# Performance work log

Hardware: AMD Instinct MI355X
Metric: run time of the kernel (lower is better)

## Reference

```python
import jax, jax.numpy as jnp
import numpy as np

INPUT_DIM = 512
HIDDEN_DIM = 512
B, N = 8, 2048


def setup_inputs() -> dict:
    key = jax.random.key(0)
    ks = jax.random.split(key, 9)
    s_in = 1.0 / np.sqrt(INPUT_DIM)
    s_h = 1.0 / np.sqrt(HIDDEN_DIM)
    return {
        "X": jax.random.normal(ks[0], (B, N, INPUT_DIM), dtype=jnp.float32),
        "Wq": jax.random.uniform(ks[1], (INPUT_DIM, HIDDEN_DIM), minval=-s_in, maxval=s_in),
        "bq": jnp.zeros((HIDDEN_DIM,), jnp.float32),
        "Wk": jax.random.uniform(ks[2], (INPUT_DIM, HIDDEN_DIM), minval=-s_in, maxval=s_in),
        "bk": jnp.zeros((HIDDEN_DIM,), jnp.float32),
        "Wv": jax.random.uniform(ks[3], (INPUT_DIM, HIDDEN_DIM), minval=-s_in, maxval=s_in),
        "bv": jnp.zeros((HIDDEN_DIM,), jnp.float32),
        "Wo": jax.random.uniform(ks[4], (HIDDEN_DIM, INPUT_DIM), minval=-s_h, maxval=s_h),
        "bo": jnp.zeros((INPUT_DIM,), jnp.float32),
        "ln_gamma": jnp.ones((INPUT_DIM,), jnp.float32),
        "ln_beta": jnp.zeros((INPUT_DIM,), jnp.float32),
    }


def reference(X, Wq, bq, Wk, bk, Wv, bv, Wo, bo, ln_gamma, ln_beta):
    q = X @ Wq + bq                      # [B,N,H]
    k = X @ Wk + bk
    v = X @ Wv + bv
    scores = jnp.einsum('bnh,bmh->bnm', q, k) / jnp.sqrt(jnp.float32(HIDDEN_DIM))
    attn = jax.nn.softmax(scores, axis=-1)      # [B,N,N]
    ctx = jnp.einsum('bnm,bmh->bnh', attn, v)   # [B,N,H]
    out = ctx @ Wo + bo + X                      # residual
    mu = jnp.mean(out, axis=-1, keepdims=True)
    var = jnp.var(out, axis=-1, keepdims=True)
    normed = (out - mu) / jnp.sqrt(var + 1e-5)
    return normed * ln_gamma + ln_beta
```

## Files before the change

### kernel.cpp

```cpp
#include <hip/hip_runtime.h>
#include <cstdint>
#include <cstddef>


typedef __bf16 bf16x8 __attribute__((ext_vector_type(8)));
typedef float  f32x4  __attribute__((ext_vector_type(4)));

__device__ __forceinline__ uint16_t f2bf(float f) {
  union { float f; uint32_t u; } v; v.f = f;
  uint32_t r = v.u + 0x7FFFu + ((v.u >> 16) & 1u);
  return (uint16_t)(r >> 16);
}

__device__ __forceinline__ void gld16(const uint16_t* g, uint16_t* l) {
  __builtin_amdgcn_global_load_lds(
      (__attribute__((address_space(1))) void*)(g),
      (__attribute__((address_space(3))) void*)(l), 16, 0, 0);
}

template <int MODE, int BM, int BN>
__global__ __launch_bounds__(512, 2) void gemm2_k(
    const uint16_t* __restrict__ A, const uint16_t* __restrict__ Bt,
    void* __restrict__ OutA, uint16_t* __restrict__ OutK,
    uint16_t* __restrict__ OutVT, float* __restrict__ rsum, int K, int lda,
    int ldb, const float* __restrict__ b0, const float* __restrict__ b1,
    const float* __restrict__ b2, float scale) {
  constexpr int MT = (BM / 2) / 16;
  constexpr int NT = (BN / 4) / 16;
  constexpr int AI = BM / 64;
  constexpr int BI = BN / 64;
  static_assert(NT == 4, "BN must be 256");
  __shared__ alignas(16) uint16_t As[2][BM * 64];
  __shared__ alignas(16) uint16_t Bs[2][BN * 64];

  const int tid = threadIdx.x;
  const int w = tid >> 6, lane = tid & 63;
  const int wm = w >> 2, wn = w & 3;

  const int gx = gridDim.x, gy = gridDim.y;
  const int nwg = gx * gy * gridDim.z;
  const int hw = blockIdx.x + gx * (blockIdx.y + gy * blockIdx.z);
  const int lg = (hw & 7) * (nwg >> 3) + (hw >> 3);
  const int bx = lg % gx, byz = lg / gx;
  const int by = byz % gy, z = byz / gy;

  const int m0 = by * BM, n0 = bx * BN;

  const uint16_t* Ab = A;
  const uint16_t* Bb = Bt;
  if (MODE == 1) { Ab += (size_t)z * 2048 * 512;  Bb += (size_t)z * 2048 * 512; }
  if (MODE == 2) { Ab += (size_t)z * 2048 * 2048; Bb += (size_t)z * 512 * 2048; }

  const int l3 = lane >> 3, l7 = lane & 7;
  const int csw = (l7 ^ l3) * 8;
  const uint16_t* gA = Ab + (size_t)(m0 + w * (BM / 8) + l3) * lda + csw;
  const uint16_t* gB = Bb + (size_t)(n0 + w * (BN / 8) + l3) * ldb + csw;

  auto stage = [&](int t, int b) {
    const int k0 = t * 64;
#pragma unroll
    for (int j = 0; j < AI; j++)
      gld16(gA + k0 + (size_t)(j * 8) * lda,
            &As[b][(w * (BM / 8) + j * 8) * 64]);
#pragma unroll
    for (int j = 0; j < BI; j++)
      gld16(gB + k0 + (size_t)(j * 8) * ldb,
            &Bs[b][(w * (BN / 8) + j * 8) * 64]);
  };

  f32x4 acc[MT][NT];
#pragma unroll
  for (int i = 0; i < MT; i++)
#pragma unroll
    for (int j = 0; j < NT; j++) acc[i][j] = (f32x4){0.f, 0.f, 0.f, 0.f};

  const int lr = lane & 15, q4 = lane >> 4;
  const int rc0 = ((q4) ^ (lr & 7)) * 8;
  const int rc1 = ((4 + q4) ^ (lr & 7)) * 8;

  const int NK = K >> 6;

  stage(0, 0);
  asm volatile("s_waitcnt vmcnt(0)" ::: "memory");
  __builtin_amdgcn_s_barrier();

  int cur = 0;
  for (int t = 0; t < NK; ++t) {
    if (t + 1 < NK) stage(t + 1, cur ^ 1);
#pragma unroll
    for (int ks = 0; ks < 2; ks++) {
      const int rc = ks ? rc1 : rc0;
      bf16x8 af[MT], bfr[NT];
#pragma unroll
      for (int mt = 0; mt < MT; mt++)
        af[mt] = *(const bf16x8*)
            &As[cur][(wm * (BM / 2) + mt * 16 + lr) * 64 + rc];
#pragma unroll
      for (int nt = 0; nt < NT; nt++)
        bfr[nt] = *(const bf16x8*)&Bs[cur][(wn * 64 + nt * 16 + lr) * 64 + rc];
#pragma unroll
      for (int nt = 0; nt < NT; nt++)
#pragma unroll
        for (int mt = 0; mt < MT; mt++)
          acc[mt][nt] = __builtin_amdgcn_mfma_f32_16x16x32_bf16(
              af[mt], bfr[nt], acc[mt][nt], 0, 0, 0);
    }
    if (t + 1 < NK) {
      asm volatile("s_waitcnt lgkmcnt(0)" ::: "memory");
      asm volatile("s_waitcnt vmcnt(0)" ::: "memory");
      __builtin_amdgcn_s_barrier();
      cur ^= 1;
    }
  }

  if (MODE == 1) {
    uint16_t* Sp = (uint16_t*)OutA + (size_t)z * 2048 * 2048;
#pragma unroll
    for (int mt = 0; mt < MT; mt++) {
      float rp[4] = {0.f, 0.f, 0.f, 0.f};
#pragma unroll
      for (int nt = 0; nt < NT; nt++) {
#pragma unroll
        for (int i = 0; i < 4; i++) {
          const int row = m0 + wm * (BM / 2) + mt * 16 + q4 * 4 + i;
          const int col = n0 + wn * 64 + nt * 16 + lr;
          const float e = __expf(acc[mt][nt][i] * scale);
          Sp[(size_t)row * 2048 + col] = f2bf(e);
          rp[i] += e;
        }
      }
#pragma unroll
      for (int i = 0; i < 4; i++) {
        float p = rp[i];
        p += __shfl_xor(p, 1); p += __shfl_xor(p, 2);
        p += __shfl_xor(p, 4); p += __shfl_xor(p, 8);
        if (lr == 0) {
          const int row = m0 + wm * (BM / 2) + mt * 16 + q4 * 4 + i;
          atomicAdd(&rsum[z * 2048 + row], p);
        }
      }
    }
  } else if (MODE == 2) {
#pragma unroll
    for (int mt = 0; mt < MT; mt++) {
#pragma unroll
      for (int i = 0; i < 4; i++) {
        const int row = m0 + wm * (BM / 2) + mt * 16 + q4 * 4 + i;
        const float sc = 1.0f / rsum[z * 2048 + row];
#pragma unroll
        for (int nt = 0; nt < NT; nt++) {
          const int col = n0 + wn * 64 + nt * 16 + lr;
          ((uint16_t*)OutA)[((size_t)z * 2048 + row) * 512 + col] =
              f2bf(acc[mt][nt][i] * sc);
        }
      }
    }
  } else {
#pragma unroll
    for (int mt = 0; mt < MT; mt++) {
#pragma unroll
      for (int nt = 0; nt < NT; nt++) {
#pragma unroll
        for (int i = 0; i < 4; i++) {
          const int row = m0 + wm * (BM / 2) + mt * 16 + q4 * 4 + i;
          const int col = n0 + wn * 64 + nt * 16 + lr;
          const float v = acc[mt][nt][i];
          const int which = col >> 9, c = col & 511;
          if (which == 0) {
            ((uint16_t*)OutA)[(size_t)row * 512 + c] = f2bf(v + b0[c]);
          } else if (which == 1) {
            OutK[(size_t)row * 512 + c] = f2bf(v + b1[c]);
          } else {
            OutVT[(size_t)(row >> 11) * (512 * 2048) + (size_t)c * 2048 +
                  (row & 2047)] = f2bf(v + b2[c]);
          }
        }
      }
    }
  }
}

template <int MODE, int BM, int BN, int WM, int WN>
__global__ __launch_bounds__(512, 4) void gemm_k(
    const uint16_t* __restrict__ A, const uint16_t* __restrict__ Bt,
    void* __restrict__ OutA, float* __restrict__ rsum, int K, int lda,
    int ldb, const float* __restrict__ b0, const float* __restrict__ b1,
    const float* __restrict__ b2, const float* __restrict__ Xres) {
  constexpr int MT = (BM / WM) / 16;
  constexpr int NT = (BN / WN) / 16;
  static_assert(MT == 4 && NT == 4, "wave tile must be 64x64");
  constexpr int AI = (BM >= 128) ? BM / 128 : 1;
  constexpr int BI = BN / 128;
  constexpr int PW = AI + BI;
  __shared__ alignas(16) uint16_t As[3][BM * 32];
  __shared__ alignas(16) uint16_t Bs[3][BN * 32];

  const int tid = threadIdx.x;
  const int w = tid >> 6, lane = tid & 63;
  const int wm = w / WN, wn = w % WN;

  const int gx = gridDim.x, gy = gridDim.y;
  const int nwg = gx * gy * gridDim.z;
  const int hw = blockIdx.x + gx * (blockIdx.y + gy * blockIdx.z);
  const int lg = (hw & 7) * (nwg >> 3) + (hw >> 3);
  const int bx = lg % gx, byz = lg / gx;
  const int by = byz % gy;

  const int m0 = by * BM, n0 = bx * BN;

  const uint16_t* Ab = A;
  const uint16_t* Bb = Bt;

  const int kc = (((lane & 3) ^ ((lane >> 2) & 3) ^ (lane >> 4)) * 8);
  const int rbA = (BM >= 128) ? w * (BM / 8) : (w & 3) * 16;
  const int rbB = w * (BN / 8);
  const uint16_t* gA = Ab + (size_t)(m0 + rbA + (lane >> 2)) * lda + kc;
  const uint16_t* gB = Bb + (size_t)(n0 + rbB + (lane >> 2)) * ldb + kc;

  f32x4 acc[MT][NT];
#pragma unroll
  for (int i = 0; i < MT; i++)
#pragma unroll
    for (int j = 0; j < NT; j++) acc[i][j] = (f32x4){0.f, 0.f, 0.f, 0.f};

  const int lr = lane & 15, q4 = lane >> 4;
  const int swz = (((lane >> 4) ^ (lr & 3) ^ (lr >> 2)) * 8);
  const int iters = K >> 5;

  auto stage = [&](int t, int buf) {
    const int k0 = t * 32;
#pragma unroll
    for (int j = 0; j < AI; j++)
      gld16(gA + k0 + (size_t)(j * 16) * lda, &As[buf][(rbA + j * 16) * 32]);
#pragma unroll
    for (int j = 0; j < BI; j++)
      gld16(gB + k0 + (size_t)(j * 16) * ldb, &Bs[buf][(rbB + j * 16) * 32]);
  };

  auto compute = [&](int buf) {
    bf16x8 af[MT], bfr[NT];
#pragma unroll
    for (int t = 0; t < MT; t++)
      af[t] = *(const bf16x8*)&As[buf][(wm * (BM / WM) + t * 16 + lr) * 32 + swz];
#pragma unroll
    for (int t = 0; t < NT; t++)
      bfr[t] = *(const bf16x8*)&Bs[buf][(wn * (BN / WN) + t * 16 + lr) * 32 + swz];
#pragma unroll
    for (int nt = 0; nt < NT; nt++)
#pragma unroll
      for (int mt = 0; mt < MT; mt++)
        acc[mt][nt] = __builtin_amdgcn_mfma_f32_16x16x32_bf16(
            af[mt], bfr[nt], acc[mt][nt], 0, 0, 0);
  };

  stage(0, 0);
  stage(1, 1);
  int buf = 0;
  for (int i = 0; i < iters - 1; ++i) {
    asm volatile("s_waitcnt vmcnt(%0)" ::"i"(PW) : "memory");
    __builtin_amdgcn_s_barrier();
    if (i + 2 < iters) stage(i + 2, (buf + 2 >= 3) ? buf - 1 : buf + 2);
    compute(buf);
    buf = (buf == 2) ? 0 : buf + 1;
  }
  asm volatile("s_waitcnt vmcnt(0)" ::: "memory");
  __builtin_amdgcn_s_barrier();
  compute(buf);

  __shared__ float redS[8][64];
  __shared__ float redQ[8][64];
  float* Op = (float*)OutA;
  __syncthreads();
#pragma unroll
  for (int mt = 0; mt < MT; mt++) {
#pragma unroll
    for (int i = 0; i < 4; i++) {
      const int rl = mt * 16 + q4 * 4 + i;
      const int row = m0 + rl;
      float ps = 0.f, pq = 0.f;
#pragma unroll
      for (int nt = 0; nt < NT; nt++) {
        const int col = wn * 64 + nt * 16 + lr;
        float v = acc[mt][nt][i] + b0[col] + Xres[(size_t)row * 512 + col];
        acc[mt][nt][i] = v;
        ps += v; pq += v * v;
      }
      ps += __shfl_xor(ps, 1); pq += __shfl_xor(pq, 1);
      ps += __shfl_xor(ps, 2); pq += __shfl_xor(pq, 2);
      ps += __shfl_xor(ps, 4); pq += __shfl_xor(pq, 4);
      ps += __shfl_xor(ps, 8); pq += __shfl_xor(pq, 8);
      if (lr == 0) { redS[w][rl] = ps; redQ[w][rl] = pq; }
    }
  }
  __syncthreads();
#pragma unroll
  for (int mt = 0; mt < MT; mt++) {
#pragma unroll
    for (int i = 0; i < 4; i++) {
      const int rl = mt * 16 + q4 * 4 + i;
      const int row = m0 + rl;
      float s8 = 0.f, q8 = 0.f;
#pragma unroll
      for (int ww = 0; ww < 8; ww++) { s8 += redS[ww][rl]; q8 += redQ[ww][rl]; }
      const float mean = s8 * (1.f / 512.f);
      const float var = q8 * (1.f / 512.f) - mean * mean;
      const float rstd = rsqrtf(var + 1e-5f);
#pragma unroll
      for (int nt = 0; nt < NT; nt++) {
        const int col = wn * 64 + nt * 16 + lr;
        Op[(size_t)row * 512 + col] =
            (acc[mt][nt][i] - mean) * rstd * b1[col] + b2[col];
      }
    }
  }
}

__global__ __launch_bounds__(256) void cvt_all_k(
    const float* __restrict__ X, uint16_t* __restrict__ Xb,
    const float* __restrict__ Wq, const float* __restrict__ Wk,
    const float* __restrict__ Wv, const float* __restrict__ Wo,
    uint16_t* __restrict__ Wt, float* __restrict__ rsum) {
  const int i = blockIdx.x * 256 + threadIdx.x;
  const float4 f = ((const float4*)X)[i];
  uint32_t lo = (uint32_t)f2bf(f.x) | ((uint32_t)f2bf(f.y) << 16);
  uint32_t hi = (uint32_t)f2bf(f.z) | ((uint32_t)f2bf(f.w) << 16);
  ((uint2*)Xb)[i] = make_uint2(lo, hi);
  if (i < 16384) rsum[i] = 0.f;
  if (i < 2048 * 512) {
    const int n = i >> 9, kk = i & 511;
    const int which = n >> 9, c = n & 511;
    const float* W =
        (which == 0) ? Wq : (which == 1) ? Wk : (which == 2) ? Wv : Wo;
    Wt[i] = f2bf(W[kk * 512 + c]);
  }
}

extern "C" void kernel_launch(void* const* d_in, const int* in_sizes, int n_in,
                              void* d_out, int out_size, void* d_ws,
                              size_t ws_size, hipStream_t stream) {
  const float* X     = (const float*)d_in[0];
  const float* Wq    = (const float*)d_in[1];
  const float* bq    = (const float*)d_in[2];
  const float* Wk    = (const float*)d_in[3];
  const float* bk    = (const float*)d_in[4];
  const float* Wv    = (const float*)d_in[5];
  const float* bv    = (const float*)d_in[6];
  const float* Wo    = (const float*)d_in[7];
  const float* bo    = (const float*)d_in[8];
  const float* gamma = (const float*)d_in[9];
  const float* beta  = (const float*)d_in[10];
  float* out = (float*)d_out;

  char* ws = (char*)d_ws;
  uint16_t* S    = (uint16_t*)(ws);
  uint16_t* Xb   = (uint16_t*)(ws);
  uint16_t* Wt   = (uint16_t*)(ws + 67108864);
  uint16_t* q    = (uint16_t*)(ws + 69206016);
  uint16_t* kb   = (uint16_t*)(ws + 85983232);
  uint16_t* vT   = (uint16_t*)(ws + 102760448);
  float*    rsum = (float*)(ws + 119537664);
  uint16_t* ctx  = q;

  cvt_all_k<<<dim3(8192), dim3(256), 0, stream>>>(X, Xb, Wq, Wk, Wv, Wo, Wt,
                                                  rsum);
  gemm2_k<0, 256, 256><<<dim3(6, 64, 1), dim3(512), 0, stream>>>(
      Xb, Wt, (void*)q, kb, vT, nullptr, 512, 512, 512, bq, bk, bv, 1.f);
  gemm2_k<1, 256, 256><<<dim3(8, 8, 8), dim3(512), 0, stream>>>(
      q, kb, (void*)S, nullptr, nullptr, rsum, 512, 512, 512, nullptr, nullptr,
      nullptr, 0.044194173824159216f);
  gemm2_k<2, 128, 256><<<dim3(2, 16, 8), dim3(512), 0, stream>>>(
      S, vT, (void*)ctx, nullptr, nullptr, rsum, 2048, 2048, 2048, nullptr,
      nullptr, nullptr, 1.f);
  gemm_k<4, 64, 512, 1, 8><<<dim3(1, 256, 1), dim3(512), 0, stream>>>(
      ctx, Wt + 1536 * 512, (void*)out, nullptr, 512, 512, 512, bo, gamma,
      beta, X);
}
```

Measured before the change: 338.2 us.

## Switch attention GEMMs to 256-thread blocks with 3-stage K=32 pipeline

Rewrites the three attention GEMM kernels to use 4-wave 256-thread blocks with smaller tiles (128x128, 64x128) and a triple-buffered LDS pipeline over 32-wide K slices with a new XOR swizzle. The old version used 8 waves with 256x256 tiles and double-buffered 64-wide K steps. The new one waits with vmcnt(PW) so two loads stay in flight. Grids grow accordingly for more blocks and better CU occupancy, at the cost of less data reuse per block and more barriers per K.

```diff
diff --git a/kernel.cpp b/kernel.cpp
--- a/kernel.cpp
+++ b/kernel.cpp
@@ -19,23 +19,23 @@
 }
 
 template <int MODE, int BM, int BN>
-__global__ __launch_bounds__(512, 2) void gemm2_k(
+__global__ __launch_bounds__(256, 2) void gemm_k(
     const uint16_t* __restrict__ A, const uint16_t* __restrict__ Bt,
     void* __restrict__ OutA, uint16_t* __restrict__ OutK,
     uint16_t* __restrict__ OutVT, float* __restrict__ rsum, int K, int lda,
     int ldb, const float* __restrict__ b0, const float* __restrict__ b1,
     const float* __restrict__ b2, float scale) {
-  constexpr int MT = (BM / 2) / 16;
-  constexpr int NT = (BN / 4) / 16;
+  constexpr int MT = BM / 32;
+  constexpr int NT = BN / 32;
   constexpr int AI = BM / 64;
   constexpr int BI = BN / 64;
-  static_assert(NT == 4, "BN must be 256");
-  __shared__ alignas(16) uint16_t As[2][BM * 64];
-  __shared__ alignas(16) uint16_t Bs[2][BN * 64];
+  constexpr int PW = AI + BI;
+  __shared__ alignas(16) uint16_t As[3][BM * 32];
+  __shared__ alignas(16) uint16_t Bs[3][BN * 32];
 
   const int tid = threadIdx.x;
   const int w = tid >> 6, lane = tid & 63;
-  const int wm = w >> 2, wn = w & 3;
+  const int wm = w >> 1, wn = w & 1;
 
   const int gx = gridDim.x, gy = gridDim.y;
   const int nwg = gx * gy * gridDim.z;
@@ -51,67 +51,61 @@
   if (MODE == 1) { Ab += (size_t)z * 2048 * 512;  Bb += (size_t)z * 2048 * 512; }
   if (MODE == 2) { Ab += (size_t)z * 2048 * 2048; Bb += (size_t)z * 512 * 2048; }
 
-  const int l3 = lane >> 3, l7 = lane & 7;
-  const int csw = (l7 ^ l3) * 8;
-  const uint16_t* gA = Ab + (size_t)(m0 + w * (BM / 8) + l3) * lda + csw;
-  const uint16_t* gB = Bb + (size_t)(n0 + w * (BN / 8) + l3) * ldb + csw;
-
-  auto stage = [&](int t, int b) {
-    const int k0 = t * 64;
+  const int kc = (((lane & 3) ^ ((lane >> 2) & 3) ^ (lane >> 4)) * 8);
+  const int rbA = w * (BM / 4);
+  const int rbB = w * (BN / 4);
+  const uint16_t* gA = Ab + (size_t)(m0 + rbA + (lane >> 2)) * lda + kc;
+  const uint16_t* gB = Bb + (size_t)(n0 + rbB + (lane >> 2)) * ldb + kc;
+
+  f32x4 acc[MT][NT];
+#pragma unroll
+  for (int i = 0; i < MT; i++)
+#pragma unroll
+    for (int j = 0; j < NT; j++) acc[i][j] = (f32x4){0.f, 0.f, 0.f, 0.f};
+
+  const int lr = lane & 15, q4 = lane >> 4;
+  const int swz = (((lane >> 4) ^ (lr & 3) ^ (lr >> 2)) * 8);
+  const int iters = K >> 5;
+
+  auto stage = [&](int t, int buf) {
+    const int k0 = t * 32;
 #pragma unroll
     for (int j = 0; j < AI; j++)
-      gld16(gA + k0 + (size_t)(j * 8) * lda,
-            &As[b][(w * (BM / 8) + j * 8) * 64]);
+      gld16(gA + k0 + (size_t)(j * 16) * lda, &As[buf][(rbA + j * 16) * 32]);
 #pragma unroll
     for (int j = 0; j < BI; j++)
-      gld16(gB + k0 + (size_t)(j * 8) * ldb,
-            &Bs[b][(w * (BN / 8) + j * 8) * 64]);
+      gld16(gB + k0 + (size_t)(j * 16) * ldb, &Bs[buf][(rbB + j * 16) * 32]);
   };
 
-  f32x4 acc[MT][NT];
-#pragma unroll
-  for (int i = 0; i < MT; i++)
-#pragma unroll
-    for (int j = 0; j < NT; j++) acc[i][j] = (f32x4){0.f, 0.f, 0.f, 0.f};
-
-  const int lr = lane & 15, q4 = lane >> 4;
-  const int rc0 = ((q4) ^ (lr & 7)) * 8;
-  const int rc1 = ((4 + q4) ^ (lr & 7)) * 8;
-
-  const int NK = K >> 6;
+  auto compute = [&](int buf) {
+    bf16x8 af[MT], bfr[NT];
+#pragma unroll
+    for (int t = 0; t < MT; t++)
+      af[t] = *(const bf16x8*)&As[buf][(wm * (BM / 2) + t * 16 + lr) * 32 + swz];
+#pragma unroll
+    for (int t = 0; t < NT; t++)
+      bfr[t] = *(const bf16x8*)&Bs[buf][(wn * (BN / 2) + t * 16 + lr) * 32 + swz];
+#pragma unroll
+    for (int nt = 0; nt < NT; nt++)
+#pragma unroll
+      for (int mt = 0; mt < MT; mt++)
+        acc[mt][nt] = __builtin_amdgcn_mfma_f32_16x16x32_bf16(
+            af[mt], bfr[nt], acc[mt][nt], 0, 0, 0);
+  };
 
   stage(0, 0);
+  stage(1, 1);
+  int buf = 0;
+  for (int i = 0; i < iters - 1; ++i) {
+    asm volatile("s_waitcnt vmcnt(%0)" ::"i"(PW) : "memory");
+    __builtin_amdgcn_s_barrier();
+    if (i + 2 < iters) stage(i + 2, (buf + 2 >= 3) ? buf - 1 : buf + 2);
+    compute(buf);
+    buf = (buf == 2) ? 0 : buf + 1;
+  }
   asm volatile("s_waitcnt vmcnt(0)" ::: "memory");
   __builtin_amdgcn_s_barrier();
-
-  int cur = 0;
-  for (int t = 0; t < NK; ++t) {
-    if (t + 1 < NK) stage(t + 1, cur ^ 1);
-#pragma unroll
-    for (int ks = 0; ks < 2; ks++) {
-      const int rc = ks ? rc1 : rc0;
-      bf16x8 af[MT], bfr[NT];
-#pragma unroll
-      for (int mt = 0; mt < MT; mt++)
-        af[mt] = *(const bf16x8*)
-            &As[cur][(wm * (BM / 2) + mt * 16 + lr) * 64 + rc];
-#pragma unroll
-      for (int nt = 0; nt < NT; nt++)
-        bfr[nt] = *(const bf16x8*)&Bs[cur][(wn * 64 + nt * 16 + lr) * 64 + rc];
-#pragma unroll
-      for (int nt = 0; nt < NT; nt++)
-#pragma unroll
-        for (int mt = 0; mt < MT; mt++)
-          acc[mt][nt] = __builtin_amdgcn_mfma_f32_16x16x32_bf16(
-              af[mt], bfr[nt], acc[mt][nt], 0, 0, 0);
-    }
-    if (t + 1 < NK) {
-      asm volatile("s_waitcnt lgkmcnt(0)" ::: "memory");
-      asm volatile("s_waitcnt vmcnt(0)" ::: "memory");
-      __builtin_amdgcn_s_barrier();
-      cur ^= 1;
-    }
-  }
+  compute(buf);
 
   if (MODE == 1) {
     uint16_t* Sp = (uint16_t*)OutA + (size_t)z * 2048 * 2048;
@@ -123,7 +117,7 @@
 #pragma unroll
         for (int i = 0; i < 4; i++) {
           const int row = m0 + wm * (BM / 2) + mt * 16 + q4 * 4 + i;
-          const int col = n0 + wn * 64 + nt * 16 + lr;
+          const int col = n0 + wn * (BN / 2) + nt * 16 + lr;
           const float e = __expf(acc[mt][nt][i] * scale);
           Sp[(size_t)row * 2048 + col] = f2bf(e);
           rp[i] += e;
@@ -149,7 +143,7 @@
         const float sc = 1.0f / rsum[z * 2048 + row];
 #pragma unroll
         for (int nt = 0; nt < NT; nt++) {
-          const int col = n0 + wn * 64 + nt * 16 + lr;
+          const int col = n0 + wn * (BN / 2) + nt * 16 + lr;
           ((uint16_t*)OutA)[((size_t)z * 2048 + row) * 512 + col] =
               f2bf(acc[mt][nt][i] * sc);
         }
@@ -163,7 +157,7 @@
 #pragma unroll
         for (int i = 0; i < 4; i++) {
           const int row = m0 + wm * (BM / 2) + mt * 16 + q4 * 4 + i;
-          const int col = n0 + wn * 64 + nt * 16 + lr;
+          const int col = n0 + wn * (BN / 2) + nt * 16 + lr;
           const float v = acc[mt][nt][i];
           const int which = col >> 9, c = col & 511;
           if (which == 0) {
@@ -180,11 +174,11 @@
   }
 }
 
-template <int MODE, int BM, int BN, int WM, int WN>
-__global__ __launch_bounds__(512, 4) void gemm_k(
+template <int BM, int BN, int WM, int WN>
+__global__ __launch_bounds__(512, 4) void gemmf_k(
     const uint16_t* __restrict__ A, const uint16_t* __restrict__ Bt,
-    void* __restrict__ OutA, float* __restrict__ rsum, int K, int lda,
-    int ldb, const float* __restrict__ b0, const float* __restrict__ b1,
+    void* __restrict__ OutA, int K, int lda, int ldb,
+    const float* __restrict__ b0, const float* __restrict__ b1,
     const float* __restrict__ b2, const float* __restrict__ Xres) {
   constexpr int MT = (BM / WM) / 16;
   constexpr int NT = (BN / WN) / 16;
@@ -363,15 +357,14 @@
 
   cvt_all_k<<<dim3(8192), dim3(256), 0, stream>>>(X, Xb, Wq, Wk, Wv, Wo, Wt,
                                                   rsum);
-  gemm2_k<0, 256, 256><<<dim3(6, 64, 1), dim3(512), 0, stream>>>(
+  gemm_k<0, 128, 128><<<dim3(12, 128, 1), dim3(256), 0, stream>>>(
       Xb, Wt, (void*)q, kb, vT, nullptr, 512, 512, 512, bq, bk, bv, 1.f);
-  gemm2_k<1, 256, 256><<<dim3(8, 8, 8), dim3(512), 0, stream>>>(
+  gemm_k<1, 128, 128><<<dim3(16, 16, 8), dim3(256), 0, stream>>>(
       q, kb, (void*)S, nullptr, nullptr, rsum, 512, 512, 512, nullptr, nullptr,
       nullptr, 0.044194173824159216f);
-  gemm2_k<2, 128, 256><<<dim3(2, 16, 8), dim3(512), 0, stream>>>(
+  gemm_k<2, 64, 128><<<dim3(4, 32, 8), dim3(256), 0, stream>>>(
       S, vT, (void*)ctx, nullptr, nullptr, rsum, 2048, 2048, 2048, nullptr,
       nullptr, nullptr, 1.f);
-  gemm_k<4, 64, 512, 1, 8><<<dim3(1, 256, 1), dim3(512), 0, stream>>>(
-      ctx, Wt + 1536 * 512, (void*)out, nullptr, 512, 512, 512, bo, gamma,
-      beta, X);
-}
+  gemmf_k<64, 512, 1, 8><<<dim3(1, 256, 1), dim3(512), 0, stream>>>(
+      ctx, Wt + 1536 * 512, (void*)out, 512, 512, 512, bo, gamma, beta, X);
+}
```

Measured after the change: 320.1 us. -5.4%, faster.
